# Performance work log

Measured on AMD Instinct MI355X. Metric: run time of the kernel, lower is better.

## Reference

```python
import jax, jax.numpy as jnp
import numpy as np

D_K = 64  # per-head key dim, used for 1/sqrt(d_k) scaling


def setup_inputs() -> dict:
    key = jax.random.key(0)
    ks = jax.random.split(key, 9)
    B, S, D, H, DK, DV = 2, 4096, 512, 8, 64, 64
    s = 0.02
    return {
        "x": jax.random.normal(ks[0], (B, S, D), dtype=jnp.float32),
        "Wq": jax.random.normal(ks[1], (H, D, DK), dtype=jnp.float32) * s,
        "bq": jax.random.normal(ks[2], (H, DK), dtype=jnp.float32) * s,
        "Wk": jax.random.normal(ks[3], (H, D, DK), dtype=jnp.float32) * s,
        "bk": jax.random.normal(ks[4], (H, DK), dtype=jnp.float32) * s,
        "Wv": jax.random.normal(ks[5], (H, D, DV), dtype=jnp.float32) * s,
        "bv": jax.random.normal(ks[6], (H, DV), dtype=jnp.float32) * s,
        "Wo": jax.random.normal(ks[7], (H * DV, D), dtype=jnp.float32) * s,
        "bo": jax.random.normal(ks[8], (D,), dtype=jnp.float32) * s,
    }


def reference(x, Wq, bq, Wk, bk, Wv, bv, Wo, bo):
    # Per-head projections, vectorized over heads: [B,H,S,dk/dv]
    q = jnp.einsum("bsd,hdk->bhsk", x, Wq) + bq[None, :, None, :]
    k = jnp.einsum("bsd,hdk->bhsk", x, Wk) + bk[None, :, None, :]
    v = jnp.einsum("bsd,hdv->bhsv", x, Wv) + bv[None, :, None, :]
    # Scaled dot-product attention (no mask; dropout inactive at eval)
    scores = jnp.einsum("bhsk,bhtk->bhst", q, k) / jnp.sqrt(jnp.float32(D_K))
    attn = jax.nn.softmax(scores, axis=-1)
    o = jnp.einsum("bhst,bhtv->bhsv", attn, v)
    # Concat heads along feature dim: [B,S,H*dv]
    B, H, S, DV = o.shape
    concat = jnp.transpose(o, (0, 2, 1, 3)).reshape(B, S, H * DV)
    return concat @ Wo + bo
```

## Files before the change

kernel.cpp:

```cpp
#include <hip/hip_runtime.h>
#include <hip/hip_bf16.h>

typedef __attribute__((ext_vector_type(8))) short bf16x8;
typedef __attribute__((ext_vector_type(4))) float f32x4;
typedef __attribute__((ext_vector_type(16))) float f32x16;
typedef __attribute__((ext_vector_type(4))) unsigned short u16x4;
typedef __attribute__((ext_vector_type(4))) unsigned int u32x4;

#define NB 2
#define NS 4096
#define ND 512
#define NH 8

__device__ __forceinline__ unsigned short f2bf(float f) {
  unsigned int u = __float_as_uint(f);
  u += 0x7fffu + ((u >> 16) & 1u);
  return (unsigned short)(u >> 16);
}

__device__ __forceinline__ float exp2_hw(float x) {
  float r;
  asm("v_exp_f32 %0, %1" : "=v"(r) : "v"(x));
  return r;
}

__device__ __forceinline__ unsigned cvtpk(float lo, float hi) {
  unsigned r;
  asm("v_cvt_pk_bf16_f32 %0, %1, %2" : "=v"(r) : "v"(lo), "v"(hi));
  return r;
}

__device__ __forceinline__ void swap32(unsigned& a, unsigned& b) {
  asm("v_permlane32_swap_b32 %0, %1" : "+v"(a), "+v"(b));
}

__device__ __forceinline__ bf16x8 mkfrag(unsigned w0, unsigned w1,
                                         unsigned w2, unsigned w3) {
  u32x4 u = {w0, w1, w2, w3};
  return __builtin_bit_cast(bf16x8, u);
}

__global__ void pack_kernel(const float* __restrict__ x,
                            const float* __restrict__ Wq,
                            const float* __restrict__ Wk,
                            const float* __restrict__ Wv,
                            const float* __restrict__ Wo,
                            unsigned short* __restrict__ x_bf,
                            unsigned short* __restrict__ w3,
                            unsigned short* __restrict__ wo_t)
{
  int idx = blockIdx.x * 256 + threadIdx.x;
  const int NX4 = NB * NS * ND / 4;
  const int NW = 512 * 512;
  if (idx < NX4) {
    const float4 f = ((const float4*)x)[idx];
    u16x4 o;
    o[0] = f2bf(f.x); o[1] = f2bf(f.y); o[2] = f2bf(f.z); o[3] = f2bf(f.w);
    ((u16x4*)x_bf)[idx] = o;
  } else if (idx < NX4 + 3 * NW) {
    int j = idx - NX4;
    int p = j / NW;
    int r = j - p * NW;
    int n = r >> 9, d = r & 511;
    int h = n >> 6, o = n & 63;
    const float* W = (p == 0) ? Wq : (p == 1) ? Wk : Wv;
    w3[j] = f2bf(W[(h * 512 + d) * 64 + o]);
  } else if (idx < NX4 + 4 * NW) {
    int j = idx - NX4 - 3 * NW;
    int n = j >> 9, kk = j & 511;
    wo_t[j] = f2bf(Wo[kk * 512 + n]);
  }
}

template <int MODE>
__global__ void gemm_bt(const unsigned short* __restrict__ A,
                        const unsigned short* __restrict__ Bm,
                        const float* __restrict__ b0,
                        const float* __restrict__ b1,
                        const float* __restrict__ b2,
                        unsigned short* __restrict__ qo,
                        unsigned short* __restrict__ ko,
                        unsigned short* __restrict__ vo,
                        float* __restrict__ fo) {
  __shared__ unsigned short Al[128 * 32];
  __shared__ unsigned short Bl[128 * 32];
  const int t = threadIdx.x;
  const int m0 = blockIdx.x * 128;
  const int n0 = blockIdx.y * 128;
  const int lane = t & 63;
  const int w = t >> 6;
  const int wm = w >> 1, wn = w & 1;
  const int c = lane & 15, g = lane >> 4;

  f32x4 acc[4][4];
#pragma unroll
  for (int i = 0; i < 4; ++i)
#pragma unroll
    for (int j = 0; j < 4; ++j) acc[i][j] = (f32x4){0.f, 0.f, 0.f, 0.f};

  const int srow = t >> 1, sseg = (t & 1) * 16;
  const unsigned short* Ap = A + (size_t)(m0 + srow) * 512 + sseg;
  const unsigned short* Bp = Bm + (size_t)(n0 + srow) * 512 + sseg;
  unsigned short* Alp = &Al[srow * 32 + sseg];
  unsigned short* Blp = &Bl[srow * 32 + sseg];

  for (int k0 = 0; k0 < 512; k0 += 32) {
    bf16x8 ra0 = *(const bf16x8*)(Ap + k0);
    bf16x8 ra1 = *(const bf16x8*)(Ap + k0 + 8);
    bf16x8 rb0 = *(const bf16x8*)(Bp + k0);
    bf16x8 rb1 = *(const bf16x8*)(Bp + k0 + 8);
    __syncthreads();
    *(bf16x8*)(Alp) = ra0;
    *(bf16x8*)(Alp + 8) = ra1;
    *(bf16x8*)(Blp) = rb0;
    *(bf16x8*)(Blp + 8) = rb1;
    __syncthreads();
    bf16x8 af[4], bfr[4];
#pragma unroll
    for (int mf = 0; mf < 4; ++mf)
      af[mf] = *(const bf16x8*)&Al[(wm * 64 + mf * 16 + c) * 32 + g * 8];
#pragma unroll
    for (int nf = 0; nf < 4; ++nf)
      bfr[nf] = *(const bf16x8*)&Bl[(wn * 64 + nf * 16 + c) * 32 + g * 8];
#pragma unroll
    for (int mf = 0; mf < 4; ++mf)
#pragma unroll
      for (int nf = 0; nf < 4; ++nf)
        acc[mf][nf] = __builtin_amdgcn_mfma_f32_16x16x32_bf16(
            af[mf], bfr[nf], acc[mf][nf], 0, 0, 0);
  }

  if (MODE == 0) {
    const int proj = n0 >> 9;
    const float* bias = proj == 0 ? b0 : (proj == 1 ? b1 : b2);
    unsigned short* dst01 = proj == 0 ? qo : ko;
    const float scale = proj == 0 ? 0.18033688011112042f : 1.0f;
#pragma unroll
    for (int nf = 0; nf < 4; ++nf) {
      const int col5 = (n0 + wn * 64 + nf * 16 + c) & 511;
      const int h = col5 >> 6, o = col5 & 63;
      const float bb = bias[col5];
#pragma unroll
      for (int mf = 0; mf < 4; ++mf) {
#pragma unroll
        for (int r = 0; r < 4; ++r) {
          const int m = m0 + wm * 64 + mf * 16 + g * 4 + r;
          const int b = m >> 12, s = m & 4095;
          const unsigned short hb = f2bf((acc[mf][nf][r] + bb) * scale);
          if (proj < 2)
            dst01[((size_t)((b * NH + h) * NS + s)) * 64 + o] = hb;
          else
            vo[((size_t)((b * NH + h) * 64 + o)) * NS + s] = hb;
        }
      }
    }
  } else {
#pragma unroll
    for (int nf = 0; nf < 4; ++nf) {
      const int col = n0 + wn * 64 + nf * 16 + c;
      const float bb = b0[col];
#pragma unroll
      for (int mf = 0; mf < 4; ++mf) {
#pragma unroll
        for (int r = 0; r < 4; ++r) {
          const int m = m0 + wm * 64 + mf * 16 + g * 4 + r;
          fo[(size_t)m * 512 + col] = acc[mf][nf][r] + bb;
        }
      }
    }
  }
}

__global__ __launch_bounds__(256, 2) void attn_kernel(
    const unsigned short* __restrict__ q,
    const unsigned short* __restrict__ k,
    const unsigned short* __restrict__ vt,
    unsigned short* __restrict__ cc)
{
  __shared__ unsigned short Kl[2][64 * 64];
  __shared__ unsigned short Vl[2][64 * 64];
  __shared__ unsigned short Ol[4][32][68];
  const int t = threadIdx.x;
  const int w = t >> 6, lane = t & 63;
  const int col = lane & 31, hi = lane >> 5;
  const int bh = blockIdx.y;
  const int b = bh >> 3, h = bh & 7;
  const int q0 = blockIdx.x * 128 + w * 32;

  const unsigned short* qh = q + (size_t)bh * NS * 64;
  const unsigned short* kh = k + (size_t)bh * NS * 64;
  const unsigned short* vh = vt + (size_t)bh * 64 * NS;

  bf16x8 qf[4];
#pragma unroll
  for (int c = 0; c < 4; ++c)
    qf[c] = *(const bf16x8*)&qh[(size_t)(q0 + col) * 64 + c * 16 + hi * 8];

  const int r0 = t >> 3, r1 = r0 + 32;
  const int ch = t & 7;
  const int koff0 = r0 * 64 + ((ch ^ (r0 & 7)) << 3);
  const int koff1 = r1 * 64 + ((ch ^ (r1 & 7)) << 3);

  f32x16 ot0, ot1;
#pragma unroll
  for (int r = 0; r < 16; ++r) { ot0[r] = 0.f; ot1[r] = 0.f; }
  float m_ = -1.0e30f, l_ = 0.f;

  {
    bf16x8 a0 = *(const bf16x8*)&kh[(size_t)r0 * 64 + ch * 8];
    bf16x8 a1 = *(const bf16x8*)&kh[(size_t)r1 * 64 + ch * 8];
    bf16x8 v0 = *(const bf16x8*)&vh[(size_t)r0 * NS + ch * 8];
    bf16x8 v1 = *(const bf16x8*)&vh[(size_t)r1 * NS + ch * 8];
    *(bf16x8*)&Kl[0][koff0] = a0;
    *(bf16x8*)&Kl[0][koff1] = a1;
    *(bf16x8*)&Vl[0][koff0] = v0;
    *(bf16x8*)&Vl[0][koff1] = v1;
    __syncthreads();
  }

  const int NT = NS / 64;
  for (int it = 0; it < NT; ++it) {
    const int cur = it & 1;
    bf16x8 pk0, pk1, pv0, pv1;
    if (it + 1 < NT) {
      const int tn = (it + 1) * 64;
      pk0 = *(const bf16x8*)&kh[(size_t)(tn + r0) * 64 + ch * 8];
      pk1 = *(const bf16x8*)&kh[(size_t)(tn + r1) * 64 + ch * 8];
      pv0 = *(const bf16x8*)&vh[(size_t)r0 * NS + tn + ch * 8];
      pv1 = *(const bf16x8*)&vh[(size_t)r1 * NS + tn + ch * 8];
    }

    f32x16 p0, p1;
#pragma unroll
    for (int r = 0; r < 16; ++r) { p0[r] = 0.f; p1[r] = 0.f; }
#pragma unroll
    for (int c = 0; c < 4; ++c) {
      const int cidx = (((2 * c + hi) ^ (col & 7)) << 3);
      bf16x8 kf0 = *(const bf16x8*)&Kl[cur][col * 64 + cidx];
      bf16x8 kf1 = *(const bf16x8*)&Kl[cur][(col + 32) * 64 + cidx];
      p0 = __builtin_amdgcn_mfma_f32_32x32x16_bf16(kf0, qf[c], p0, 0, 0, 0);
      p1 = __builtin_amdgcn_mfma_f32_32x32x16_bf16(kf1, qf[c], p1, 0, 0, 0);
    }

    float mx[8];
#pragma unroll
    for (int r = 0; r < 8; ++r)
      mx[r] = fmaxf(fmaxf(p0[r], p0[r + 8]), fmaxf(p1[r], p1[r + 8]));
#pragma unroll
    for (int s = 4; s >= 1; s >>= 1)
#pragma unroll
      for (int r = 0; r < 8; ++r)
        if (r < s) mx[r] = fmaxf(mx[r], mx[r + s]);
    float pm = mx[0];
    pm = fmaxf(pm, __shfl_xor(pm, 32, 64));
    if (__any(pm > m_ + 8.f)) {
      const float resc = exp2_hw(m_ - pm);
      m_ = pm;
      l_ *= resc;
#pragma unroll
      for (int r = 0; r < 16; ++r) { ot0[r] *= resc; ot1[r] *= resc; }
    }
    float e0[16], e1[16];
#pragma unroll
    for (int r = 0; r < 16; ++r) {
      e0[r] = exp2_hw(p0[r] - m_);
      e1[r] = exp2_hw(p1[r] - m_);
    }
    float sm[8];
#pragma unroll
    for (int r = 0; r < 8; ++r)
      sm[r] = (e0[r] + e0[r + 8]) + (e1[r] + e1[r + 8]);
#pragma unroll
    for (int s = 4; s >= 1; s >>= 1)
#pragma unroll
      for (int r = 0; r < 8; ++r)
        if (r < s) sm[r] += sm[r + s];
    float rs = sm[0];
    rs += __shfl_xor(rs, 32, 64);
    l_ += rs;

    unsigned g0[8], g1[8];
#pragma unroll
    for (int gg = 0; gg < 8; ++gg) {
      g0[gg] = cvtpk(e0[2 * gg], e0[2 * gg + 1]);
      g1[gg] = cvtpk(e1[2 * gg], e1[2 * gg + 1]);
    }
    bf16x8 pb[4];
    {
      unsigned a, c2, b2, d2;
      a = g0[0]; b2 = g0[2]; swap32(a, b2);
      c2 = g0[1]; d2 = g0[3]; swap32(c2, d2);
      pb[0] = mkfrag(a, c2, b2, d2);
      a = g0[4]; b2 = g0[6]; swap32(a, b2);
      c2 = g0[5]; d2 = g0[7]; swap32(c2, d2);
      pb[1] = mkfrag(a, c2, b2, d2);
      a = g1[0]; b2 = g1[2]; swap32(a, b2);
      c2 = g1[1]; d2 = g1[3]; swap32(c2, d2);
      pb[2] = mkfrag(a, c2, b2, d2);
      a = g1[4]; b2 = g1[6]; swap32(a, b2);
      c2 = g1[5]; d2 = g1[7]; swap32(c2, d2);
      pb[3] = mkfrag(a, c2, b2, d2);
    }

#pragma unroll
    for (int ks = 0; ks < 4; ++ks) {
      const int cidx = (((2 * ks + hi) ^ (col & 7)) << 3);
      bf16x8 vf0 = *(const bf16x8*)&Vl[cur][col * 64 + cidx];
      bf16x8 vf1 = *(const bf16x8*)&Vl[cur][(col + 32) * 64 + cidx];
      ot0 = __builtin_amdgcn_mfma_f32_32x32x16_bf16(vf0, pb[ks], ot0, 0, 0, 0);
      ot1 = __builtin_amdgcn_mfma_f32_32x32x16_bf16(vf1, pb[ks], ot1, 0, 0, 0);
    }

    if (it + 1 < NT) {
      __syncthreads();
      *(bf16x8*)&Kl[cur ^ 1][koff0] = pk0;
      *(bf16x8*)&Kl[cur ^ 1][koff1] = pk1;
      *(bf16x8*)&Vl[cur ^ 1][koff0] = pv0;
      *(bf16x8*)&Vl[cur ^ 1][koff1] = pv1;
      __syncthreads();
    }
  }

  const float inv = 1.0f / l_;
#pragma unroll
  for (int r = 0; r < 16; ++r) {
    const int dvb = (r & 3) + 8 * (r >> 2) + 4 * hi;
    Ol[w][col][dvb] = f2bf(ot0[r] * inv);
    Ol[w][col][dvb + 32] = f2bf(ot1[r] * inv);
  }
  asm volatile("s_waitcnt lgkmcnt(0)" ::: "memory");
  const int row = lane >> 1;
#pragma unroll
  for (int p = 0; p < 4; ++p) {
    const int chunk = (lane & 1) + 2 * p;
    bf16x8 vv = *(const bf16x8*)&Ol[w][row][chunk * 8];
    *(bf16x8*)&cc[((size_t)(b * NS + q0 + row)) * 512 + h * 64 + chunk * 8] = vv;
  }
}

extern "C" void kernel_launch(void* const* d_in, const int* in_sizes, int n_in,
                              void* d_out, int out_size, void* d_ws, size_t ws_size,
                              hipStream_t stream) {
  const float* x  = (const float*)d_in[0];
  const float* Wq = (const float*)d_in[1];
  const float* bq = (const float*)d_in[2];
  const float* Wk = (const float*)d_in[3];
  const float* bk = (const float*)d_in[4];
  const float* Wv = (const float*)d_in[5];
  const float* bv = (const float*)d_in[6];
  const float* Wo = (const float*)d_in[7];
  const float* bo = (const float*)d_in[8];

  unsigned char* ws = (unsigned char*)d_ws;
  unsigned short* x_bf = (unsigned short*)(ws);
  unsigned short* w3   = (unsigned short*)(ws + 8388608);
  unsigned short* wo_t = (unsigned short*)(ws + 9961472);
  unsigned short* qb   = (unsigned short*)(ws + 10485760);
  unsigned short* kb   = (unsigned short*)(ws + 18874368);
  unsigned short* vb   = (unsigned short*)(ws + 27262976);
  unsigned short* cc   = x_bf;

  pack_kernel<<<8192, 256, 0, stream>>>(x, Wq, Wk, Wv, Wo, x_bf, w3, wo_t);
  gemm_bt<0><<<dim3(64, 12), 256, 0, stream>>>(x_bf, w3, bq, bk, bv, qb, kb, vb,
                                               nullptr);
  attn_kernel<<<dim3(32, 16), 256, 0, stream>>>(qb, kb, vb, cc);
  gemm_bt<1><<<dim3(64, 4), 256, 0, stream>>>(cc, wo_t, bo, nullptr, nullptr,
                                              nullptr, nullptr, nullptr,
                                              (float*)d_out);
}
```

Measured before the change: 154.1 us.

## Split attention over key range in two halves and merge with combine kernel

Attention is split into two passes over halves of the key sequence, which doubles the grid from 512 to 1024 blocks so more of the device's compute units are busy. Each half writes unnormalized bf16 partial outputs plus per-row max and sum, and a new combine kernel rescales and merges them into the concat buffer. Shared memory is unioned between the K/V tiles and the output staging, and launch bounds are raised to 4 blocks per unit to allow higher occupancy. The cost is an extra kernel launch, extra global traffic for the partials, and a second bf16 rounding of the partial outputs. The split path is taken only when the workspace is large enough.

```diff
diff --git a/kernel.cpp b/kernel.cpp
--- a/kernel.cpp
+++ b/kernel.cpp
@@ -16,6 +16,10 @@
   unsigned int u = __float_as_uint(f);
   u += 0x7fffu + ((u >> 16) & 1u);
   return (unsigned short)(u >> 16);
+}
+
+__device__ __forceinline__ float bf2f(unsigned short h) {
+  return __uint_as_float(((unsigned)h) << 16);
 }
 
 __device__ __forceinline__ float exp2_hw(float x) {
@@ -171,21 +175,28 @@
   }
 }
 
-__global__ __launch_bounds__(256, 2) void attn_kernel(
+template <int SPLITS>
+__global__ __launch_bounds__(256, 4) void attn_kernel(
     const unsigned short* __restrict__ q,
     const unsigned short* __restrict__ k,
     const unsigned short* __restrict__ vt,
-    unsigned short* __restrict__ cc)
+    unsigned short* __restrict__ cc,
+    unsigned short* __restrict__ op,
+    float* __restrict__ ml)
 {
-  __shared__ unsigned short Kl[2][64 * 64];
-  __shared__ unsigned short Vl[2][64 * 64];
-  __shared__ unsigned short Ol[4][32][68];
+  union SMemU {
+    struct { unsigned short Kl[2][4096]; unsigned short Vl[2][4096]; } kv;
+    unsigned short Ol[4][32][68];
+  };
+  __shared__ SMemU sm;
   const int t = threadIdx.x;
   const int w = t >> 6, lane = t & 63;
   const int col = lane & 31, hi = lane >> 5;
-  const int bh = blockIdx.y;
+  const int bh = blockIdx.y & 15;
+  const int sp = blockIdx.y >> 4;
   const int b = bh >> 3, h = bh & 7;
   const int q0 = blockIdx.x * 128 + w * 32;
+  const int kbase = sp * (NS / SPLITS);
 
   const unsigned short* qh = q + (size_t)bh * NS * 64;
   const unsigned short* kh = k + (size_t)bh * NS * 64;
@@ -207,23 +218,23 @@
   float m_ = -1.0e30f, l_ = 0.f;
 
   {
-    bf16x8 a0 = *(const bf16x8*)&kh[(size_t)r0 * 64 + ch * 8];
-    bf16x8 a1 = *(const bf16x8*)&kh[(size_t)r1 * 64 + ch * 8];
-    bf16x8 v0 = *(const bf16x8*)&vh[(size_t)r0 * NS + ch * 8];
-    bf16x8 v1 = *(const bf16x8*)&vh[(size_t)r1 * NS + ch * 8];
-    *(bf16x8*)&Kl[0][koff0] = a0;
-    *(bf16x8*)&Kl[0][koff1] = a1;
-    *(bf16x8*)&Vl[0][koff0] = v0;
-    *(bf16x8*)&Vl[0][koff1] = v1;
+    bf16x8 a0 = *(const bf16x8*)&kh[(size_t)(kbase + r0) * 64 + ch * 8];
+    bf16x8 a1 = *(const bf16x8*)&kh[(size_t)(kbase + r1) * 64 + ch * 8];
+    bf16x8 v0 = *(const bf16x8*)&vh[(size_t)r0 * NS + kbase + ch * 8];
+    bf16x8 v1 = *(const bf16x8*)&vh[(size_t)r1 * NS + kbase + ch * 8];
+    *(bf16x8*)&sm.kv.Kl[0][koff0] = a0;
+    *(bf16x8*)&sm.kv.Kl[0][koff1] = a1;
+    *(bf16x8*)&sm.kv.Vl[0][koff0] = v0;
+    *(bf16x8*)&sm.kv.Vl[0][koff1] = v1;
     __syncthreads();
   }
 
-  const int NT = NS / 64;
+  const int NT = NS / (64 * SPLITS);
   for (int it = 0; it < NT; ++it) {
     const int cur = it & 1;
     bf16x8 pk0, pk1, pv0, pv1;
     if (it + 1 < NT) {
-      const int tn = (it + 1) * 64;
+      const int tn = kbase + (it + 1) * 64;
       pk0 = *(const bf16x8*)&kh[(size_t)(tn + r0) * 64 + ch * 8];
       pk1 = *(const bf16x8*)&kh[(size_t)(tn + r1) * 64 + ch * 8];
       pv0 = *(const bf16x8*)&vh[(size_t)r0 * NS + tn + ch * 8];
@@ -236,8 +247,8 @@
 #pragma unroll
     for (int c = 0; c < 4; ++c) {
       const int cidx = (((2 * c + hi) ^ (col & 7)) << 3);
-      bf16x8 kf0 = *(const bf16x8*)&Kl[cur][col * 64 + cidx];
-      bf16x8 kf1 = *(const bf16x8*)&Kl[cur][(col + 32) * 64 + cidx];
+      bf16x8 kf0 = *(const bf16x8*)&sm.kv.Kl[cur][col * 64 + cidx];
+      bf16x8 kf1 = *(const bf16x8*)&sm.kv.Kl[cur][(col + 32) * 64 + cidx];
       p0 = __builtin_amdgcn_mfma_f32_32x32x16_bf16(kf0, qf[c], p0, 0, 0, 0);
       p1 = __builtin_amdgcn_mfma_f32_32x32x16_bf16(kf1, qf[c], p1, 0, 0, 0);
     }
@@ -266,16 +277,16 @@
       e0[r] = exp2_hw(p0[r] - m_);
       e1[r] = exp2_hw(p1[r] - m_);
     }
-    float sm[8];
+    float smv[8];
 #pragma unroll
     for (int r = 0; r < 8; ++r)
-      sm[r] = (e0[r] + e0[r + 8]) + (e1[r] + e1[r + 8]);
+      smv[r] = (e0[r] + e0[r + 8]) + (e1[r] + e1[r + 8]);
 #pragma unroll
     for (int s = 4; s >= 1; s >>= 1)
 #pragma unroll
       for (int r = 0; r < 8; ++r)
-        if (r < s) sm[r] += sm[r + s];
-    float rs = sm[0];
+        if (r < s) smv[r] += smv[r + s];
+    float rs = smv[0];
     rs += __shfl_xor(rs, 32, 64);
     l_ += rs;
 
@@ -305,37 +316,73 @@
 #pragma unroll
     for (int ks = 0; ks < 4; ++ks) {
       const int cidx = (((2 * ks + hi) ^ (col & 7)) << 3);
-      bf16x8 vf0 = *(const bf16x8*)&Vl[cur][col * 64 + cidx];
-      bf16x8 vf1 = *(const bf16x8*)&Vl[cur][(col + 32) * 64 + cidx];
+      bf16x8 vf0 = *(const bf16x8*)&sm.kv.Vl[cur][col * 64 + cidx];
+      bf16x8 vf1 = *(const bf16x8*)&sm.kv.Vl[cur][(col + 32) * 64 + cidx];
       ot0 = __builtin_amdgcn_mfma_f32_32x32x16_bf16(vf0, pb[ks], ot0, 0, 0, 0);
       ot1 = __builtin_amdgcn_mfma_f32_32x32x16_bf16(vf1, pb[ks], ot1, 0, 0, 0);
     }
 
     if (it + 1 < NT) {
       __syncthreads();
-      *(bf16x8*)&Kl[cur ^ 1][koff0] = pk0;
-      *(bf16x8*)&Kl[cur ^ 1][koff1] = pk1;
-      *(bf16x8*)&Vl[cur ^ 1][koff0] = pv0;
-      *(bf16x8*)&Vl[cur ^ 1][koff1] = pv1;
+      *(bf16x8*)&sm.kv.Kl[cur ^ 1][koff0] = pk0;
+      *(bf16x8*)&sm.kv.Kl[cur ^ 1][koff1] = pk1;
+      *(bf16x8*)&sm.kv.Vl[cur ^ 1][koff0] = pv0;
+      *(bf16x8*)&sm.kv.Vl[cur ^ 1][koff1] = pv1;
       __syncthreads();
     }
   }
 
-  const float inv = 1.0f / l_;
+  __syncthreads();
+
+  const float inv = (SPLITS == 1) ? (1.0f / l_) : 1.0f;
 #pragma unroll
   for (int r = 0; r < 16; ++r) {
     const int dvb = (r & 3) + 8 * (r >> 2) + 4 * hi;
-    Ol[w][col][dvb] = f2bf(ot0[r] * inv);
-    Ol[w][col][dvb + 32] = f2bf(ot1[r] * inv);
+    sm.Ol[w][col][dvb] = f2bf(ot0[r] * inv);
+    sm.Ol[w][col][dvb + 32] = f2bf(ot1[r] * inv);
+  }
+  if (SPLITS == 2 && hi == 0) {
+    float2 mm = {m_, l_};
+    *(float2*)&ml[((size_t)(sp * 16 + bh) * NS + q0 + col) * 2] = mm;
   }
   asm volatile("s_waitcnt lgkmcnt(0)" ::: "memory");
   const int row = lane >> 1;
 #pragma unroll
   for (int p = 0; p < 4; ++p) {
     const int chunk = (lane & 1) + 2 * p;
-    bf16x8 vv = *(const bf16x8*)&Ol[w][row][chunk * 8];
-    *(bf16x8*)&cc[((size_t)(b * NS + q0 + row)) * 512 + h * 64 + chunk * 8] = vv;
-  }
+    bf16x8 vv = *(const bf16x8*)&sm.Ol[w][row][chunk * 8];
+    if (SPLITS == 1)
+      *(bf16x8*)&cc[((size_t)(b * NS + q0 + row)) * 512 + h * 64 + chunk * 8] = vv;
+    else
+      *(bf16x8*)&op[((size_t)(sp * 16 + bh) * NS + q0 + row) * 64 + chunk * 8] = vv;
+  }
+}
+
+__global__ void combine_kernel(const unsigned short* __restrict__ op,
+                               const float* __restrict__ ml,
+                               unsigned short* __restrict__ cc) {
+  const int id = blockIdx.x * 256 + threadIdx.x;
+  const int chunk = id & 7;
+  const int qq = (id >> 3) & 4095;
+  const int bh = id >> 15;
+  const int b = bh >> 3, h = bh & 7;
+  const float2 ml0 = *(const float2*)&ml[((size_t)bh * NS + qq) * 2];
+  const float2 ml1 = *(const float2*)&ml[((size_t)(16 + bh) * NS + qq) * 2];
+  const float m = fmaxf(ml0.x, ml1.x);
+  const float w0 = exp2_hw(ml0.x - m), w1 = exp2_hw(ml1.x - m);
+  const float invl = 1.0f / (ml0.y * w0 + ml1.y * w1);
+  const bf16x8 o0 =
+      *(const bf16x8*)&op[((size_t)bh * NS + qq) * 64 + chunk * 8];
+  const bf16x8 o1 =
+      *(const bf16x8*)&op[((size_t)(16 + bh) * NS + qq) * 64 + chunk * 8];
+  bf16x8 out;
+#pragma unroll
+  for (int j = 0; j < 8; ++j) {
+    const float v = (bf2f((unsigned short)o0[j]) * w0 +
+                     bf2f((unsigned short)o1[j]) * w1) * invl;
+    out[j] = (short)f2bf(v);
+  }
+  *(bf16x8*)&cc[((size_t)(b * NS + qq)) * 512 + h * 64 + chunk * 8] = out;
 }
 
 extern "C" void kernel_launch(void* const* d_in, const int* in_sizes, int n_in,
@@ -358,12 +405,23 @@
   unsigned short* qb   = (unsigned short*)(ws + 10485760);
   unsigned short* kb   = (unsigned short*)(ws + 18874368);
   unsigned short* vb   = (unsigned short*)(ws + 27262976);
+  unsigned short* op   = (unsigned short*)(ws + 35651584);
+  float*          mlp  = (float*)(ws + 52428800);
   unsigned short* cc   = x_bf;
+
+  const bool two_split = ws_size >= 53477376ull;
 
   pack_kernel<<<8192, 256, 0, stream>>>(x, Wq, Wk, Wv, Wo, x_bf, w3, wo_t);
   gemm_bt<0><<<dim3(64, 12), 256, 0, stream>>>(x_bf, w3, bq, bk, bv, qb, kb, vb,
                                                nullptr);
-  attn_kernel<<<dim3(32, 16), 256, 0, stream>>>(qb, kb, vb, cc);
+  if (two_split) {
+    attn_kernel<2><<<dim3(32, 32), 256, 0, stream>>>(qb, kb, vb, nullptr, op,
+                                                     mlp);
+    combine_kernel<<<2048, 256, 0, stream>>>(op, mlp, cc);
+  } else {
+    attn_kernel<1><<<dim3(32, 16), 256, 0, stream>>>(qb, kb, vb, cc, nullptr,
+                                                     nullptr);
+  }
   gemm_bt<1><<<dim3(64, 4), 256, 0, stream>>>(cc, wo_t, bo, nullptr, nullptr,
                                               nullptr, nullptr, nullptr,
                                               (float*)d_out);
```

Measured after the change: 160.6 us. 4.2% more time.
